# Performance work log

Hardware: AMD Instinct MI355X
Metric: run time of the kernel (lower is better)

The kernel has to match this reference:

```python
import jax, jax.numpy as jnp
import numpy as np

N, E = 50000, 800000          # nodes, edges
CUR, HID, OUT = 128, 128, 128  # cur_dim, hidden_dim, output_dim
NEG_SLOPE = 0.01               # F.leaky_relu default


def setup_inputs() -> dict:
    key = jax.random.key(0)
    ks = jax.random.split(key, 12)
    rn = lambda k, shp, s: jax.random.normal(k, shp, dtype=jnp.float32) * s
    s_c, s_h, s_o = 1.0 / np.sqrt(CUR), 1.0 / np.sqrt(HID), 1.0 / np.sqrt(OUT)
    return {
        "h": rn(ks[0], (N, CUR), 1.0),
        "x": rn(ks[1], (N, CUR), 1.0),
        "edge_index": jax.random.randint(ks[2], (2, E), 0, N, dtype=jnp.int32),
        "edge_weight": jax.random.uniform(ks[3], (E,), dtype=jnp.float32),
        # preprocessor_x: Linear(CUR, HID)
        "Wp": rn(ks[4], (HID, CUR), s_c), "bp": jnp.zeros((HID,), jnp.float32),
        # ChebConv(HID, OUT, K=2): two weight mats + bias
        "Wc0": rn(ks[5], (OUT, HID), s_h), "Wc1": rn(ks[6], (OUT, HID), s_h),
        "bc": jnp.zeros((OUT,), jnp.float32),
        # SAGEConv(HID, OUT): lin_rel (neighbors, with bias) + lin_root (self)
        "Wrel": rn(ks[7], (OUT, HID), s_h), "brel": jnp.zeros((OUT,), jnp.float32),
        "Wroot": rn(ks[8], (OUT, HID), s_h),
        # final Linear(OUT, OUT)
        "Wl": rn(ks[9], (OUT, OUT), s_o), "bl": jnp.zeros((OUT,), jnp.float32),
    }


def reference(h, x, edge_index, edge_weight, Wp, bp, Wc0, Wc1, bc,
              Wrel, brel, Wroot, Wl, bl):
    n = x.shape[0]
    src, dst = edge_index[0], edge_index[1]
    seg = lambda d, i: jax.ops.segment_sum(d, i, num_segments=n)

    his = x
    xh = x @ Wp.T + bp                               # [N, HID]

    # --- ChebConv, K=2, sym norm, lambda_max=2 => Lhat = -D^{-1/2} A D^{-1/2}
    deg = seg(edge_weight, src)                       # weighted degree
    dis = jnp.where(deg > 0, jax.lax.rsqrt(jnp.where(deg > 0, deg, 1.0)), 0.0)
    norm = -dis[src] * edge_weight * dis[dst]         # [E]
    Tx1 = seg(norm[:, None] * xh[src], dst)           # [N, HID]
    o1 = jax.nn.leaky_relu(xh @ Wc0.T + Tx1 @ Wc1.T + bc, NEG_SLOPE)

    # --- SAGEConv: mean of edge_weight-scaled neighbor feats + root transform
    msum = seg(edge_weight[:, None] * xh[src], dst)   # [N, HID]
    cnt = seg(jnp.ones_like(edge_weight), dst)        # in-degree
    mean = msum / jnp.maximum(cnt, 1.0)[:, None]
    o2 = jax.nn.leaky_relu(mean @ Wrel.T + brel + xh @ Wroot.T, NEG_SLOPE)

    o3 = (o1 + o2) @ Wl.T + bl
    return (his, o3)
```

## Files before the change

### kernel.cpp

```cpp
#include <hip/hip_runtime.h>

#define NN 50000
#define EE 800000
#define D  128
#define NCH 64
#define CH  12500
#define NR  8
#define RS  6250
#define KCB 512
#define KCB2 1024
#define XHB 782
#define CSB 196
#define PKB 384
#define FB  1563

typedef short short8 __attribute__((ext_vector_type(8)));
typedef float floatx4 __attribute__((ext_vector_type(4)));
typedef float floatx16 __attribute__((ext_vector_type(16)));

__device__ __forceinline__ float leaky(float v) { return v > 0.f ? v : 0.01f * v; }

__device__ __forceinline__ unsigned short f2bf(float f) {
    unsigned int u = __float_as_uint(f);
    u = (u + 0x7fff + ((u >> 16) & 1)) >> 16;
    return (unsigned short)u;
}
__device__ __forceinline__ float bf2f(unsigned int h) {
    return __uint_as_float(h << 16);
}

__global__ __launch_bounds__(256) void k_pre(
    const float* __restrict__ Wp,  const float* __restrict__ Wc0,
    const float* __restrict__ Wc1, const float* __restrict__ Wrel,
    const float* __restrict__ Wroot, const float* __restrict__ Wl,
    unsigned short* __restrict__ Pall) {
    int gid = blockIdx.x * 256 + threadIdx.x;
    int mm = gid >> 14;
    int r = gid & 16383;
    int j  = r & 7;
    int l  = (r >> 3) & 63;
    int n, k;
    if (mm == 0) {
        int ct = (r >> 9) & 7;
        int kc = r >> 12;
        n = ct * 16 + (l & 15);
        k = kc * 32 + (l >> 4) * 8 + j;
    } else {
        int ct = (r >> 9) & 3;
        int kc = (r >> 11) & 7;
        n = ct * 32 + (l & 31);
        k = kc * 16 + (l >> 5) * 8 + j;
    }
    const float* W = mm == 0 ? Wp : mm == 1 ? Wc0 : mm == 2 ? Wc1
                   : mm == 3 ? Wrel : mm == 4 ? Wroot : Wl;
    Pall[gid] = f2bf(W[n * 128 + k]);
}

__global__ __launch_bounds__(256) void k_main(
    const int* __restrict__ src, const int* __restrict__ dst,
    const float* __restrict__ ew,
    int* __restrict__ counts,
    float* __restrict__ degp,
    unsigned short* __restrict__ rank,
    const float* __restrict__ x, const float* __restrict__ bp,
    unsigned short* __restrict__ xh16, float* __restrict__ his,
    const unsigned short* __restrict__ Pall) {
    __shared__ __align__(16) unsigned int sbuf[6272];
    int b = blockIdx.x;
    if (b < KCB) {
        int c = b & 63;
        int rlo = (b >> 6) * RS;
        for (int i = threadIdx.x; i < RS / 2; i += 256) sbuf[i] = 0u;
        __syncthreads();
        int base = c * CH;
        for (int i0 = threadIdx.x * 4; i0 < CH; i0 += 1024) {
            int e = base + i0;
            int4 d4 = *(const int4*)(dst + e);
            unsigned dr;
            dr = (unsigned)(d4.x - rlo);
            if (dr < RS) {
                unsigned old = atomicAdd(&sbuf[dr >> 1], 1u << ((dr & 1) * 16));
                rank[e]     = (unsigned short)(old >> ((dr & 1) * 16));
            }
            dr = (unsigned)(d4.y - rlo);
            if (dr < RS) {
                unsigned old = atomicAdd(&sbuf[dr >> 1], 1u << ((dr & 1) * 16));
                rank[e + 1] = (unsigned short)(old >> ((dr & 1) * 16));
            }
            dr = (unsigned)(d4.z - rlo);
            if (dr < RS) {
                unsigned old = atomicAdd(&sbuf[dr >> 1], 1u << ((dr & 1) * 16));
                rank[e + 2] = (unsigned short)(old >> ((dr & 1) * 16));
            }
            dr = (unsigned)(d4.w - rlo);
            if (dr < RS) {
                unsigned old = atomicAdd(&sbuf[dr >> 1], 1u << ((dr & 1) * 16));
                rank[e + 3] = (unsigned short)(old >> ((dr & 1) * 16));
            }
        }
        __syncthreads();
        size_t ob = (size_t)c * NN + rlo;
        for (int i = threadIdx.x; i < RS; i += 256)
            counts[ob + i] = (int)((sbuf[i >> 1] >> ((i & 1) * 16)) & 0xffffu);
    } else if (b < KCB2) {
        int bb = b - KCB;
        int c = bb & 63;
        int rlo = (bb >> 6) * RS;
        float* sdeg = (float*)sbuf;
        for (int i = threadIdx.x; i < RS; i += 256) sdeg[i] = 0.f;
        __syncthreads();
        int base = c * CH;
        for (int i0 = threadIdx.x * 4; i0 < CH; i0 += 1024) {
            int e = base + i0;
            int4   s4 = *(const int4*)(src + e);
            float4 w4 = *(const float4*)(ew + e);
            unsigned sr;
            sr = (unsigned)(s4.x - rlo); if (sr < RS) atomicAdd(&sdeg[sr], w4.x);
            sr = (unsigned)(s4.y - rlo); if (sr < RS) atomicAdd(&sdeg[sr], w4.y);
            sr = (unsigned)(s4.z - rlo); if (sr < RS) atomicAdd(&sdeg[sr], w4.z);
            sr = (unsigned)(s4.w - rlo); if (sr < RS) atomicAdd(&sdeg[sr], w4.w);
        }
        __syncthreads();
        size_t ob = (size_t)c * NN + rlo;
        for (int i = threadIdx.x; i < RS; i += 256) degp[ob + i] = sdeg[i];
    } else {
        int bb = b - KCB2;
        const unsigned short* Pp = Pall;
        int wave = threadIdx.x >> 6, l = threadIdx.x & 63;
        int n0 = bb * 64 + wave * 16;
        int m = l & 15, q = l >> 4;
        int nodeA = n0 + m;
        bool av = nodeA < NN;
        int na = av ? nodeA : 0;
        floatx4 acc[8];
#pragma unroll
        for (int ct = 0; ct < 8; ++ct) acc[ct] = (floatx4)(0.f);
#pragma unroll
        for (int kc = 0; kc < 4; ++kc) {
            const float* ap = x + (size_t)na * 128 + kc * 32 + q * 8;
            float4 f0 = av ? *(const float4*)ap       : make_float4(0, 0, 0, 0);
            float4 f1 = av ? *(const float4*)(ap + 4) : make_float4(0, 0, 0, 0);
            if (av) {
                float* hp = his + (size_t)nodeA * 128 + kc * 32 + q * 8;
                *(float4*)hp       = f0;
                *(float4*)(hp + 4) = f1;
            }
            short8 a;
            a[0] = f2bf(f0.x); a[1] = f2bf(f0.y); a[2] = f2bf(f0.z); a[3] = f2bf(f0.w);
            a[4] = f2bf(f1.x); a[5] = f2bf(f1.y); a[6] = f2bf(f1.z); a[7] = f2bf(f1.w);
#pragma unroll
            for (int ct = 0; ct < 8; ++ct) {
                short8 bfr = *(const short8*)(Pp + ((kc * 8 + ct) << 9) + l * 8);
                acc[ct] = __builtin_amdgcn_mfma_f32_16x16x32_bf16(a, bfr, acc[ct], 0, 0, 0);
            }
        }
#pragma unroll
        for (int ct = 0; ct < 8; ++ct) {
            int col = ct * 16 + m;
            float bias = bp[col];
#pragma unroll
            for (int r = 0; r < 4; ++r) {
                int node = n0 + q * 4 + r;
                if (node < NN) xh16[(size_t)node * 128 + col] = f2bf(acc[ct][r] + bias);
            }
        }
    }
}

__global__ __launch_bounds__(256) void k_colscan(int* __restrict__ counts,
                                                 const float* __restrict__ degp,
                                                 int* __restrict__ cntI,
                                                 float* __restrict__ deg,
                                                 int* __restrict__ blocksum) {
    __shared__ int ws4[4];
    int t = threadIdx.x;
    int n = blockIdx.x * 256 + t;
    int acc = 0; float dacc = 0.f;
    if (n < NN) {
#pragma unroll 8
        for (int c = 0; c < NCH; ++c) {
            size_t idx = (size_t)c * NN + n;
            int v = counts[idx];
            counts[idx] = acc;
            acc += v;
            dacc += degp[idx];
        }
        cntI[n] = acc;
        deg[n] = dacc;
    }
    int s = (n < NN) ? acc : 0;
#pragma unroll
    for (int off = 32; off > 0; off >>= 1) s += __shfl_down(s, off, 64);
    if ((t & 63) == 0) ws4[t >> 6] = s;
    __syncthreads();
    if (t == 0) blocksum[blockIdx.x] = ws4[0] + ws4[1] + ws4[2] + ws4[3];
}

__global__ __launch_bounds__(256) void k_scan_mid(const int* __restrict__ blocksum,
                                                  int* __restrict__ blockoff,
                                                  int* __restrict__ rowstart) {
    __shared__ int wtot[4];
    int t = threadIdx.x, lane = t & 63, wave = t >> 6;
    int v = (t < CSB) ? blocksum[t] : 0;
    int incl = v;
#pragma unroll
    for (int off = 1; off < 64; off <<= 1) {
        int u = __shfl_up(incl, off, 64);
        if (lane >= off) incl += u;
    }
    if (lane == 63) wtot[wave] = incl;
    __syncthreads();
    int wpre = 0;
    for (int w = 0; w < wave; ++w) wpre += wtot[w];
    incl += wpre;
    if (t < CSB) blockoff[t] = incl - v;
    if (t == 255) rowstart[NN] = incl;
}

__global__ __launch_bounds__(256) void k_scan_final(const int* __restrict__ cntI,
                                                    const int* __restrict__ blockoff,
                                                    int* __restrict__ rowstart) {
    __shared__ int wtot[4];
    int t = threadIdx.x, lane = t & 63, wave = t >> 6;
    int n = blockIdx.x * 256 + t;
    int v = (n < NN) ? cntI[n] : 0;
    int incl = v;
#pragma unroll
    for (int off = 1; off < 64; off <<= 1) {
        int u = __shfl_up(incl, off, 64);
        if (lane >= off) incl += u;
    }
    if (lane == 63) wtot[wave] = incl;
    __syncthreads();
    int wpre = 0;
    for (int w = 0; w < wave; ++w) wpre += wtot[w];
    incl += wpre;
    if (n < NN) rowstart[n] = blockoff[blockIdx.x] + incl - v;
}

__global__ __launch_bounds__(256) void k_bucket(const int* __restrict__ src,
                                                const int* __restrict__ dst,
                                                const float* __restrict__ ew,
                                                const float* __restrict__ deg,
                                                const int* __restrict__ rowstart,
                                                const int* __restrict__ chunkoff,
                                                const unsigned short* __restrict__ rank,
                                                int4* __restrict__ rec) {
    int e = blockIdx.x * blockDim.x + threadIdx.x;
    if (e >= EE) return;
    int s = src[e], d = dst[e];
    float w = ew[e];
    float degs = deg[s];
    float dis_s = degs > 0.f ? rsqrtf(degs) : 0.f;
    int c = e / CH;
    int pos = rowstart[d] + chunkoff[(size_t)c * NN + d] + (int)rank[e];
    int4 r;
    r.x = s;
    r.y = __float_as_int(w);
    r.z = __float_as_int(dis_s * w);
    r.w = 0;
    rec[pos] = r;
}

__global__ __launch_bounds__(256) void k_gather(const int* __restrict__ rowstart,
                                                const int4* __restrict__ rec,
                                                const float* __restrict__ deg,
                                                const unsigned short* __restrict__ xh16,
                                                unsigned int* __restrict__ tx16,
                                                unsigned int* __restrict__ mn16) {
    int wave = threadIdx.x >> 6, l = threadIdx.x & 63;
    int n = blockIdx.x * 4 + wave;
    if (n >= NN) return;
    int lo = rowstart[n], hi = rowstart[n + 1];
    int half = l >> 5, c32 = l & 31;
    float am0 = 0.f, am1 = 0.f, am2 = 0.f, am3 = 0.f;
    float at0 = 0.f, at1 = 0.f, at2 = 0.f, at3 = 0.f;
    int e = lo + half;
    for (; e + 6 < hi; e += 8) {
        int4 r0 = rec[e], r1 = rec[e + 2], r2 = rec[e + 4], r3 = rec[e + 6];
        uint2 v0 = *(const uint2*)(xh16 + (size_t)r0.x * 128 + c32 * 4);
        uint2 v1 = *(const uint2*)(xh16 + (size_t)r1.x * 128 + c32 * 4);
        uint2 v2 = *(const uint2*)(xh16 + (size_t)r2.x * 128 + c32 * 4);
        uint2 v3 = *(const uint2*)(xh16 + (size_t)r3.x * 128 + c32 * 4);
        float w0 = __int_as_float(r0.y), u0 = __int_as_float(r0.z);
        float w1 = __int_as_float(r1.y), u1 = __int_as_float(r1.z);
        float w2 = __int_as_float(r2.y), u2 = __int_as_float(r2.z);
        float w3 = __int_as_float(r3.y), u3 = __int_as_float(r3.z);
        float a0, a1, a2, a3;
        a0 = bf2f(v0.x & 0xffff); a1 = bf2f(v0.x >> 16);
        a2 = bf2f(v0.y & 0xffff); a3 = bf2f(v0.y >> 16);
        am0 = fmaf(w0, a0, am0); am1 = fmaf(w0, a1, am1);
        am2 = fmaf(w0, a2, am2); am3 = fmaf(w0, a3, am3);
        at0 = fmaf(u0, a0, at0); at1 = fmaf(u0, a1, at1);
        at2 = fmaf(u0, a2, at2); at3 = fmaf(u0, a3, at3);
        a0 = bf2f(v1.x & 0xffff); a1 = bf2f(v1.x >> 16);
        a2 = bf2f(v1.y & 0xffff); a3 = bf2f(v1.y >> 16);
        am0 = fmaf(w1, a0, am0); am1 = fmaf(w1, a1, am1);
        am2 = fmaf(w1, a2, am2); am3 = fmaf(w1, a3, am3);
        at0 = fmaf(u1, a0, at0); at1 = fmaf(u1, a1, at1);
        at2 = fmaf(u1, a2, at2); at3 = fmaf(u1, a3, at3);
        a0 = bf2f(v2.x & 0xffff); a1 = bf2f(v2.x >> 16);
        a2 = bf2f(v2.y & 0xffff); a3 = bf2f(v2.y >> 16);
        am0 = fmaf(w2, a0, am0); am1 = fmaf(w2, a1, am1);
        am2 = fmaf(w2, a2, am2); am3 = fmaf(w2, a3, am3);
        at0 = fmaf(u2, a0, at0); at1 = fmaf(u2, a1, at1);
        at2 = fmaf(u2, a2, at2); at3 = fmaf(u2, a3, at3);
        a0 = bf2f(v3.x & 0xffff); a1 = bf2f(v3.x >> 16);
        a2 = bf2f(v3.y & 0xffff); a3 = bf2f(v3.y >> 16);
        am0 = fmaf(w3, a0, am0); am1 = fmaf(w3, a1, am1);
        am2 = fmaf(w3, a2, am2); am3 = fmaf(w3, a3, am3);
        at0 = fmaf(u3, a0, at0); at1 = fmaf(u3, a1, at1);
        at2 = fmaf(u3, a2, at2); at3 = fmaf(u3, a3, at3);
    }
    for (; e < hi; e += 2) {
        int4 r0 = rec[e];
        uint2 v0 = *(const uint2*)(xh16 + (size_t)r0.x * 128 + c32 * 4);
        float w0 = __int_as_float(r0.y), u0 = __int_as_float(r0.z);
        float a0 = bf2f(v0.x & 0xffff), a1 = bf2f(v0.x >> 16);
        float a2 = bf2f(v0.y & 0xffff), a3 = bf2f(v0.y >> 16);
        am0 = fmaf(w0, a0, am0); am1 = fmaf(w0, a1, am1);
        am2 = fmaf(w0, a2, am2); am3 = fmaf(w0, a3, am3);
        at0 = fmaf(u0, a0, at0); at1 = fmaf(u0, a1, at1);
        at2 = fmaf(u0, a2, at2); at3 = fmaf(u0, a3, at3);
    }
    am0 += __shfl_xor(am0, 32, 64); am1 += __shfl_xor(am1, 32, 64);
    am2 += __shfl_xor(am2, 32, 64); am3 += __shfl_xor(am3, 32, 64);
    at0 += __shfl_xor(at0, 32, 64); at1 += __shfl_xor(at1, 32, 64);
    at2 += __shfl_xor(at2, 32, 64); at3 += __shfl_xor(at3, 32, 64);
    float dd = deg[n];
    float dis_d = dd > 0.f ? rsqrtf(dd) : 0.f;
    int c = hi - lo;
    float ic = 1.f / (float)(c > 0 ? c : 1);
    if (half == 0) {
        uint2 t;
        t.x = (unsigned int)f2bf(-dis_d * at0) | ((unsigned int)f2bf(-dis_d * at1) << 16);
        t.y = (unsigned int)f2bf(-dis_d * at2) | ((unsigned int)f2bf(-dis_d * at3) << 16);
        *(uint2*)(tx16 + (size_t)n * 64 + c32 * 2) = t;
    } else {
        uint2 m;
        m.x = (unsigned int)f2bf(am0 * ic) | ((unsigned int)f2bf(am1 * ic) << 16);
        m.y = (unsigned int)f2bf(am2 * ic) | ((unsigned int)f2bf(am3 * ic) << 16);
        *(uint2*)(mn16 + (size_t)n * 64 + c32 * 2) = m;
    }
}

__global__ __launch_bounds__(256, 4) void k_fused(const unsigned short* __restrict__ xh16,
                                               const unsigned short* __restrict__ tx16,
                                               const unsigned short* __restrict__ mn16,
                                               const unsigned short* __restrict__ Pall,
                                               const float* __restrict__ bc,
                                               const float* __restrict__ brel,
                                               const float* __restrict__ bl,
                                               float* __restrict__ out) {
    const unsigned short* Pc0  = Pall + 1 * 16384;
    const unsigned short* Pc1  = Pall + 2 * 16384;
    const unsigned short* Prel = Pall + 3 * 16384;
    const unsigned short* Proot= Pall + 4 * 16384;
    const unsigned short* Pl   = Pall + 5 * 16384;
    __shared__ __align__(16) unsigned short sS[32][128];
    int ct = threadIdx.x >> 6, l = threadIdx.x & 63;
    int n0 = blockIdx.x * 32;
    int row = l & 31, half = l >> 5;
    int node = n0 + row;
    bool av = node < NN;
    size_t ra = (size_t)(av ? node : 0) * 128 + half * 8;
    floatx16 acc1 = (floatx16)(0.f), acc2 = (floatx16)(0.f);
#pragma unroll
    for (int kc = 0; kc < 8; ++kc) {
        short8 Axh = *(const short8*)(xh16 + ra + kc * 16);
        short8 Atx = *(const short8*)(tx16 + ra + kc * 16);
        short8 Amn = *(const short8*)(mn16 + ra + kc * 16);
        int po = ((kc * 4 + ct) << 9) + l * 8;
        short8 b0 = *(const short8*)(Pc0 + po);
        short8 b1 = *(const short8*)(Pc1 + po);
        short8 b2 = *(const short8*)(Prel + po);
        short8 b3 = *(const short8*)(Proot + po);
        acc1 = __builtin_amdgcn_mfma_f32_32x32x16_bf16(Axh, b0, acc1, 0, 0, 0);
        acc1 = __builtin_amdgcn_mfma_f32_32x32x16_bf16(Atx, b1, acc1, 0, 0, 0);
        acc2 = __builtin_amdgcn_mfma_f32_32x32x16_bf16(Amn, b2, acc2, 0, 0, 0);
        acc2 = __builtin_amdgcn_mfma_f32_32x32x16_bf16(Axh, b3, acc2, 0, 0, 0);
    }
    int col = ct * 32 + row;
    float b1v = bc[col], b2v = brel[col];
#pragma unroll
    for (int r = 0; r < 16; ++r) {
        int rr = (r & 3) + 8 * (r >> 2) + 4 * half;
        float u = leaky(acc1[r] + b1v) + leaky(acc2[r] + b2v);
        int sw = ((((col >> 3) ^ rr) & 15) << 3) | (col & 7);
        sS[rr][sw] = f2bf(u);
    }
    __syncthreads();
    floatx16 acc3 = (floatx16)(0.f);
#pragma unroll
    for (int kc = 0; kc < 8; ++kc) {
        int g = (kc * 2 + half) ^ (row & 15);
        short8 As = *(const short8*)&sS[row][g << 3];
        short8 b = *(const short8*)(Pl + ((kc * 4 + ct) << 9) + l * 8);
        acc3 = __builtin_amdgcn_mfma_f32_32x32x16_bf16(As, b, acc3, 0, 0, 0);
    }
    float bv = bl[col];
#pragma unroll
    for (int r = 0; r < 16; ++r) {
        int rr = (r & 3) + 8 * (r >> 2) + 4 * half;
        int nd = n0 + rr;
        if (nd < NN) out[(size_t)nd * 128 + col] = acc3[r] + bv;
    }
}

extern "C" void kernel_launch(void* const* d_in, const int* in_sizes, int n_in,
                              void* d_out, int out_size, void* d_ws, size_t ws_size,
                              hipStream_t stream) {
    const float* x    = (const float*)d_in[1];
    const int*   ei   = (const int*)d_in[2];
    const float* ew   = (const float*)d_in[3];
    const float* Wp   = (const float*)d_in[4];
    const float* bp   = (const float*)d_in[5];
    const float* Wc0  = (const float*)d_in[6];
    const float* Wc1  = (const float*)d_in[7];
    const float* bc   = (const float*)d_in[8];
    const float* Wrel = (const float*)d_in[9];
    const float* brel = (const float*)d_in[10];
    const float* Wroot= (const float*)d_in[11];
    const float* Wl   = (const float*)d_in[12];
    const float* bl   = (const float*)d_in[13];
    (void)in_sizes; (void)n_in; (void)out_size; (void)ws_size;
    float* out = (float*)d_out;

    unsigned short* xh16 = (unsigned short*)d_ws;
    unsigned short* tx16 = xh16 + (size_t)NN * 128;
    unsigned short* mn16 = tx16 + (size_t)NN * 128;
    unsigned short* Pall = mn16 + (size_t)NN * 128;
    int*   counts = (int*)(Pall + 6 * 16384);
    int4*  rec    = (int4*)(counts + (size_t)NCH * NN);
    float* degp   = (float*)rec;
    unsigned short* rank = (unsigned short*)(rec + EE);
    int*   rowstart = (int*)(rank + EE);
    int*   blocksum = rowstart + NN + 2;
    int*   blockoff = blocksum + CSB;
    int*   cntI   = blockoff + CSB;
    float* deg    = (float*)(cntI + NN);

    const int* srcI = ei;
    const int* dstI = ei + EE;

    k_pre<<<PKB, 256, 0, stream>>>(Wp, Wc0, Wc1, Wrel, Wroot, Wl, Pall);
    k_main<<<KCB2 + XHB, 256, 0, stream>>>(
        srcI, dstI, ew, counts, degp, rank, x, bp, xh16, out, Pall);
    k_colscan<<<CSB, 256, 0, stream>>>(counts, degp, cntI, deg, blocksum);
    k_scan_mid<<<1, 256, 0, stream>>>(blocksum, blockoff, rowstart);
    k_scan_final<<<CSB, 256, 0, stream>>>(cntI, blockoff, rowstart);
    k_bucket<<<(EE + 255) / 256, 256, 0, stream>>>(srcI, dstI, ew, deg, rowstart,
                                                   counts, rank, rec);
    k_gather<<<(NN + 3) / 4, 256, 0, stream>>>(rowstart, rec, deg, xh16,
                                               (unsigned int*)tx16, (unsigned int*)mn16);
    k_fused<<<FB, 256, 0, stream>>>(xh16, tx16, mn16, Pall,
                                    bc, brel, bl, out + (size_t)NN * 128);
}
```

Measured before the change: 246.1 us.

## Fuse neighbor gather into MFMA epilogue kernel and merge scan kernels

The CSR gather that builds the Chebyshev and mean-aggregated features now runs inside the fused MFMA kernel. Each block aggregates its 32 nodes into swizzled shared-memory tiles instead of writing tx16/mn16 to global memory and reading them back. Separately, the mid-level block-sum scan is folded into the final scan kernel, with every block redundantly scanning the 196 block sums. Together this drops two launches and one global round-trip of intermediate features. The cost is fewer waves doing the latency-bound gather per node, since 1563 blocks now each walk 8 nodes per wave serially, and extra shared memory that may lower occupancy.

```diff
diff --git a/kernel.cpp b/kernel.cpp
--- a/kernel.cpp
+++ b/kernel.cpp
@@ -196,12 +196,29 @@
     if (t == 0) blocksum[blockIdx.x] = ws4[0] + ws4[1] + ws4[2] + ws4[3];
 }
 
-__global__ __launch_bounds__(256) void k_scan_mid(const int* __restrict__ blocksum,
-                                                  int* __restrict__ blockoff,
-                                                  int* __restrict__ rowstart) {
+__global__ __launch_bounds__(256) void k_scan_final(const int* __restrict__ cntI,
+                                                    const int* __restrict__ blocksum,
+                                                    int* __restrict__ rowstart) {
+    __shared__ int sbs[256];
     __shared__ int wtot[4];
     int t = threadIdx.x, lane = t & 63, wave = t >> 6;
-    int v = (t < CSB) ? blocksum[t] : 0;
+    int bv = (t < CSB) ? blocksum[t] : 0;
+    int binc = bv;
+#pragma unroll
+    for (int off = 1; off < 64; off <<= 1) {
+        int u = __shfl_up(binc, off, 64);
+        if (lane >= off) binc += u;
+    }
+    if (lane == 63) wtot[wave] = binc;
+    __syncthreads();
+    int bpre = 0;
+    for (int w = 0; w < wave; ++w) bpre += wtot[w];
+    sbs[t] = binc + bpre;
+    __syncthreads();
+    int boff = (blockIdx.x == 0) ? 0 : sbs[blockIdx.x - 1];
+    if (blockIdx.x == 0 && t == 0) rowstart[NN] = sbs[CSB - 1];
+    int n = blockIdx.x * 256 + t;
+    int v = (n < NN) ? cntI[n] : 0;
     int incl = v;
 #pragma unroll
     for (int off = 1; off < 64; off <<= 1) {
@@ -213,29 +230,7 @@
     int wpre = 0;
     for (int w = 0; w < wave; ++w) wpre += wtot[w];
     incl += wpre;
-    if (t < CSB) blockoff[t] = incl - v;
-    if (t == 255) rowstart[NN] = incl;
-}
-
-__global__ __launch_bounds__(256) void k_scan_final(const int* __restrict__ cntI,
-                                                    const int* __restrict__ blockoff,
-                                                    int* __restrict__ rowstart) {
-    __shared__ int wtot[4];
-    int t = threadIdx.x, lane = t & 63, wave = t >> 6;
-    int n = blockIdx.x * 256 + t;
-    int v = (n < NN) ? cntI[n] : 0;
-    int incl = v;
-#pragma unroll
-    for (int off = 1; off < 64; off <<= 1) {
-        int u = __shfl_up(incl, off, 64);
-        if (lane >= off) incl += u;
-    }
-    if (lane == 63) wtot[wave] = incl;
-    __syncthreads();
-    int wpre = 0;
-    for (int w = 0; w < wave; ++w) wpre += wtot[w];
-    incl += wpre;
-    if (n < NN) rowstart[n] = blockoff[blockIdx.x] + incl - v;
+    if (n < NN) rowstart[n] = boff + incl - v;
 }
 
 __global__ __launch_bounds__(256) void k_bucket(const int* __restrict__ src,
@@ -262,91 +257,10 @@
     rec[pos] = r;
 }
 
-__global__ __launch_bounds__(256) void k_gather(const int* __restrict__ rowstart,
-                                                const int4* __restrict__ rec,
-                                                const float* __restrict__ deg,
-                                                const unsigned short* __restrict__ xh16,
-                                                unsigned int* __restrict__ tx16,
-                                                unsigned int* __restrict__ mn16) {
-    int wave = threadIdx.x >> 6, l = threadIdx.x & 63;
-    int n = blockIdx.x * 4 + wave;
-    if (n >= NN) return;
-    int lo = rowstart[n], hi = rowstart[n + 1];
-    int half = l >> 5, c32 = l & 31;
-    float am0 = 0.f, am1 = 0.f, am2 = 0.f, am3 = 0.f;
-    float at0 = 0.f, at1 = 0.f, at2 = 0.f, at3 = 0.f;
-    int e = lo + half;
-    for (; e + 6 < hi; e += 8) {
-        int4 r0 = rec[e], r1 = rec[e + 2], r2 = rec[e + 4], r3 = rec[e + 6];
-        uint2 v0 = *(const uint2*)(xh16 + (size_t)r0.x * 128 + c32 * 4);
-        uint2 v1 = *(const uint2*)(xh16 + (size_t)r1.x * 128 + c32 * 4);
-        uint2 v2 = *(const uint2*)(xh16 + (size_t)r2.x * 128 + c32 * 4);
-        uint2 v3 = *(const uint2*)(xh16 + (size_t)r3.x * 128 + c32 * 4);
-        float w0 = __int_as_float(r0.y), u0 = __int_as_float(r0.z);
-        float w1 = __int_as_float(r1.y), u1 = __int_as_float(r1.z);
-        float w2 = __int_as_float(r2.y), u2 = __int_as_float(r2.z);
-        float w3 = __int_as_float(r3.y), u3 = __int_as_float(r3.z);
-        float a0, a1, a2, a3;
-        a0 = bf2f(v0.x & 0xffff); a1 = bf2f(v0.x >> 16);
-        a2 = bf2f(v0.y & 0xffff); a3 = bf2f(v0.y >> 16);
-        am0 = fmaf(w0, a0, am0); am1 = fmaf(w0, a1, am1);
-        am2 = fmaf(w0, a2, am2); am3 = fmaf(w0, a3, am3);
-        at0 = fmaf(u0, a0, at0); at1 = fmaf(u0, a1, at1);
-        at2 = fmaf(u0, a2, at2); at3 = fmaf(u0, a3, at3);
-        a0 = bf2f(v1.x & 0xffff); a1 = bf2f(v1.x >> 16);
-        a2 = bf2f(v1.y & 0xffff); a3 = bf2f(v1.y >> 16);
-        am0 = fmaf(w1, a0, am0); am1 = fmaf(w1, a1, am1);
-        am2 = fmaf(w1, a2, am2); am3 = fmaf(w1, a3, am3);
-        at0 = fmaf(u1, a0, at0); at1 = fmaf(u1, a1, at1);
-        at2 = fmaf(u1, a2, at2); at3 = fmaf(u1, a3, at3);
-        a0 = bf2f(v2.x & 0xffff); a1 = bf2f(v2.x >> 16);
-        a2 = bf2f(v2.y & 0xffff); a3 = bf2f(v2.y >> 16);
-        am0 = fmaf(w2, a0, am0); am1 = fmaf(w2, a1, am1);
-        am2 = fmaf(w2, a2, am2); am3 = fmaf(w2, a3, am3);
-        at0 = fmaf(u2, a0, at0); at1 = fmaf(u2, a1, at1);
-        at2 = fmaf(u2, a2, at2); at3 = fmaf(u2, a3, at3);
-        a0 = bf2f(v3.x & 0xffff); a1 = bf2f(v3.x >> 16);
-        a2 = bf2f(v3.y & 0xffff); a3 = bf2f(v3.y >> 16);
-        am0 = fmaf(w3, a0, am0); am1 = fmaf(w3, a1, am1);
-        am2 = fmaf(w3, a2, am2); am3 = fmaf(w3, a3, am3);
-        at0 = fmaf(u3, a0, at0); at1 = fmaf(u3, a1, at1);
-        at2 = fmaf(u3, a2, at2); at3 = fmaf(u3, a3, at3);
-    }
-    for (; e < hi; e += 2) {
-        int4 r0 = rec[e];
-        uint2 v0 = *(const uint2*)(xh16 + (size_t)r0.x * 128 + c32 * 4);
-        float w0 = __int_as_float(r0.y), u0 = __int_as_float(r0.z);
-        float a0 = bf2f(v0.x & 0xffff), a1 = bf2f(v0.x >> 16);
-        float a2 = bf2f(v0.y & 0xffff), a3 = bf2f(v0.y >> 16);
-        am0 = fmaf(w0, a0, am0); am1 = fmaf(w0, a1, am1);
-        am2 = fmaf(w0, a2, am2); am3 = fmaf(w0, a3, am3);
-        at0 = fmaf(u0, a0, at0); at1 = fmaf(u0, a1, at1);
-        at2 = fmaf(u0, a2, at2); at3 = fmaf(u0, a3, at3);
-    }
-    am0 += __shfl_xor(am0, 32, 64); am1 += __shfl_xor(am1, 32, 64);
-    am2 += __shfl_xor(am2, 32, 64); am3 += __shfl_xor(am3, 32, 64);
-    at0 += __shfl_xor(at0, 32, 64); at1 += __shfl_xor(at1, 32, 64);
-    at2 += __shfl_xor(at2, 32, 64); at3 += __shfl_xor(at3, 32, 64);
-    float dd = deg[n];
-    float dis_d = dd > 0.f ? rsqrtf(dd) : 0.f;
-    int c = hi - lo;
-    float ic = 1.f / (float)(c > 0 ? c : 1);
-    if (half == 0) {
-        uint2 t;
-        t.x = (unsigned int)f2bf(-dis_d * at0) | ((unsigned int)f2bf(-dis_d * at1) << 16);
-        t.y = (unsigned int)f2bf(-dis_d * at2) | ((unsigned int)f2bf(-dis_d * at3) << 16);
-        *(uint2*)(tx16 + (size_t)n * 64 + c32 * 2) = t;
-    } else {
-        uint2 m;
-        m.x = (unsigned int)f2bf(am0 * ic) | ((unsigned int)f2bf(am1 * ic) << 16);
-        m.y = (unsigned int)f2bf(am2 * ic) | ((unsigned int)f2bf(am3 * ic) << 16);
-        *(uint2*)(mn16 + (size_t)n * 64 + c32 * 2) = m;
-    }
-}
-
-__global__ __launch_bounds__(256, 4) void k_fused(const unsigned short* __restrict__ xh16,
-                                               const unsigned short* __restrict__ tx16,
-                                               const unsigned short* __restrict__ mn16,
+__global__ __launch_bounds__(256, 4) void k_gf(const int* __restrict__ rowstart,
+                                               const int4* __restrict__ rec,
+                                               const float* __restrict__ deg,
+                                               const unsigned short* __restrict__ xh16,
                                                const unsigned short* __restrict__ Pall,
                                                const float* __restrict__ bc,
                                                const float* __restrict__ brel,
@@ -357,19 +271,102 @@
     const unsigned short* Prel = Pall + 3 * 16384;
     const unsigned short* Proot= Pall + 4 * 16384;
     const unsigned short* Pl   = Pall + 5 * 16384;
+    __shared__ __align__(16) unsigned short sTX[32][128];
+    __shared__ __align__(16) unsigned short sMN[32][128];
     __shared__ __align__(16) unsigned short sS[32][128];
-    int ct = threadIdx.x >> 6, l = threadIdx.x & 63;
+    int w = threadIdx.x >> 6, l = threadIdx.x & 63;
     int n0 = blockIdx.x * 32;
-    int row = l & 31, half = l >> 5;
+    int half = l >> 5, c32 = l & 31;
+    for (int i = 0; i < 8; ++i) {
+        int rr = w * 8 + i;
+        int n = n0 + rr;
+        int lo = 0, hi = 0;
+        if (n < NN) { lo = rowstart[n]; hi = rowstart[n + 1]; }
+        float am0 = 0.f, am1 = 0.f, am2 = 0.f, am3 = 0.f;
+        float at0 = 0.f, at1 = 0.f, at2 = 0.f, at3 = 0.f;
+        int e = lo + half;
+        for (; e + 6 < hi; e += 8) {
+            int4 r0 = rec[e], r1 = rec[e + 2], r2 = rec[e + 4], r3 = rec[e + 6];
+            uint2 v0 = *(const uint2*)(xh16 + (size_t)r0.x * 128 + c32 * 4);
+            uint2 v1 = *(const uint2*)(xh16 + (size_t)r1.x * 128 + c32 * 4);
+            uint2 v2 = *(const uint2*)(xh16 + (size_t)r2.x * 128 + c32 * 4);
+            uint2 v3 = *(const uint2*)(xh16 + (size_t)r3.x * 128 + c32 * 4);
+            float w0 = __int_as_float(r0.y), u0 = __int_as_float(r0.z);
+            float w1 = __int_as_float(r1.y), u1 = __int_as_float(r1.z);
+            float w2 = __int_as_float(r2.y), u2 = __int_as_float(r2.z);
+            float w3 = __int_as_float(r3.y), u3 = __int_as_float(r3.z);
+            float a0, a1, a2, a3;
+            a0 = bf2f(v0.x & 0xffff); a1 = bf2f(v0.x >> 16);
+            a2 = bf2f(v0.y & 0xffff); a3 = bf2f(v0.y >> 16);
+            am0 = fmaf(w0, a0, am0); am1 = fmaf(w0, a1, am1);
+            am2 = fmaf(w0, a2, am2); am3 = fmaf(w0, a3, am3);
+            at0 = fmaf(u0, a0, at0); at1 = fmaf(u0, a1, at1);
+            at2 = fmaf(u0, a2, at2); at3 = fmaf(u0, a3, at3);
+            a0 = bf2f(v1.x & 0xffff); a1 = bf2f(v1.x >> 16);
+            a2 = bf2f(v1.y & 0xffff); a3 = bf2f(v1.y >> 16);
+            am0 = fmaf(w1, a0, am0); am1 = fmaf(w1, a1, am1);
+            am2 = fmaf(w1, a2, am2); am3 = fmaf(w1, a3, am3);
+            at0 = fmaf(u1, a0, at0); at1 = fmaf(u1, a1, at1);
+            at2 = fmaf(u1, a2, at2); at3 = fmaf(u1, a3, at3);
+            a0 = bf2f(v2.x & 0xffff); a1 = bf2f(v2.x >> 16);
+            a2 = bf2f(v2.y & 0xffff); a3 = bf2f(v2.y >> 16);
+            am0 = fmaf(w2, a0, am0); am1 = fmaf(w2, a1, am1);
+            am2 = fmaf(w2, a2, am2); am3 = fmaf(w2, a3, am3);
+            at0 = fmaf(u2, a0, at0); at1 = fmaf(u2, a1, at1);
+            at2 = fmaf(u2, a2, at2); at3 = fmaf(u2, a3, at3);
+            a0 = bf2f(v3.x & 0xffff); a1 = bf2f(v3.x >> 16);
+            a2 = bf2f(v3.y & 0xffff); a3 = bf2f(v3.y >> 16);
+            am0 = fmaf(w3, a0, am0); am1 = fmaf(w3, a1, am1);
+            am2 = fmaf(w3, a2, am2); am3 = fmaf(w3, a3, am3);
+            at0 = fmaf(u3, a0, at0); at1 = fmaf(u3, a1, at1);
+            at2 = fmaf(u3, a2, at2); at3 = fmaf(u3, a3, at3);
+        }
+        for (; e < hi; e += 2) {
+            int4 r0 = rec[e];
+            uint2 v0 = *(const uint2*)(xh16 + (size_t)r0.x * 128 + c32 * 4);
+            float w0 = __int_as_float(r0.y), u0 = __int_as_float(r0.z);
+            float a0 = bf2f(v0.x & 0xffff), a1 = bf2f(v0.x >> 16);
+            float a2 = bf2f(v0.y & 0xffff), a3 = bf2f(v0.y >> 16);
+            am0 = fmaf(w0, a0, am0); am1 = fmaf(w0, a1, am1);
+            am2 = fmaf(w0, a2, am2); am3 = fmaf(w0, a3, am3);
+            at0 = fmaf(u0, a0, at0); at1 = fmaf(u0, a1, at1);
+            at2 = fmaf(u0, a2, at2); at3 = fmaf(u0, a3, at3);
+        }
+        am0 += __shfl_xor(am0, 32, 64); am1 += __shfl_xor(am1, 32, 64);
+        am2 += __shfl_xor(am2, 32, 64); am3 += __shfl_xor(am3, 32, 64);
+        at0 += __shfl_xor(at0, 32, 64); at1 += __shfl_xor(at1, 32, 64);
+        at2 += __shfl_xor(at2, 32, 64); at3 += __shfl_xor(at3, 32, 64);
+        float dd = (n < NN) ? deg[n] : 0.f;
+        float dis_d = dd > 0.f ? rsqrtf(dd) : 0.f;
+        int c = hi - lo;
+        float ic = 1.f / (float)(c > 0 ? c : 1);
+        int cb = c32 * 4;
+        int sw = ((((cb >> 3) ^ (rr & 15)) & 15) << 3) | (cb & 7);
+        if (half == 0) {
+            uint2 tv;
+            tv.x = (unsigned int)f2bf(-dis_d * at0) | ((unsigned int)f2bf(-dis_d * at1) << 16);
+            tv.y = (unsigned int)f2bf(-dis_d * at2) | ((unsigned int)f2bf(-dis_d * at3) << 16);
+            *(uint2*)&sTX[rr][sw] = tv;
+        } else {
+            uint2 mv;
+            mv.x = (unsigned int)f2bf(am0 * ic) | ((unsigned int)f2bf(am1 * ic) << 16);
+            mv.y = (unsigned int)f2bf(am2 * ic) | ((unsigned int)f2bf(am3 * ic) << 16);
+            *(uint2*)&sMN[rr][sw] = mv;
+        }
+    }
+    __syncthreads();
+    int ct = w;
+    int row = l & 31;
     int node = n0 + row;
     bool av = node < NN;
     size_t ra = (size_t)(av ? node : 0) * 128 + half * 8;
     floatx16 acc1 = (floatx16)(0.f), acc2 = (floatx16)(0.f);
 #pragma unroll
     for (int kc = 0; kc < 8; ++kc) {
+        int g = ((kc * 2 + half) ^ (row & 15)) & 15;
         short8 Axh = *(const short8*)(xh16 + ra + kc * 16);
-        short8 Atx = *(const short8*)(tx16 + ra + kc * 16);
-        short8 Amn = *(const short8*)(mn16 + ra + kc * 16);
+        short8 Atx = *(const short8*)&sTX[row][g << 3];
+        short8 Amn = *(const short8*)&sMN[row][g << 3];
         int po = ((kc * 4 + ct) << 9) + l * 8;
         short8 b0 = *(const short8*)(Pc0 + po);
         short8 b1 = *(const short8*)(Pc1 + po);
@@ -447,12 +444,9 @@
     k_main<<<KCB2 + XHB, 256, 0, stream>>>(
         srcI, dstI, ew, counts, degp, rank, x, bp, xh16, out, Pall);
     k_colscan<<<CSB, 256, 0, stream>>>(counts, degp, cntI, deg, blocksum);
-    k_scan_mid<<<1, 256, 0, stream>>>(blocksum, blockoff, rowstart);
-    k_scan_final<<<CSB, 256, 0, stream>>>(cntI, blockoff, rowstart);
+    k_scan_final<<<CSB, 256, 0, stream>>>(cntI, blocksum, rowstart);
     k_bucket<<<(EE + 255) / 256, 256, 0, stream>>>(srcI, dstI, ew, deg, rowstart,
                                                    counts, rank, rec);
-    k_gather<<<(NN + 3) / 4, 256, 0, stream>>>(rowstart, rec, deg, xh16,
-                                               (unsigned int*)tx16, (unsigned int*)mn16);
-    k_fused<<<FB, 256, 0, stream>>>(xh16, tx16, mn16, Pall,
-                                    bc, brel, bl, out + (size_t)NN * 128);
-}
+    k_gf<<<FB, 256, 0, stream>>>(rowstart, rec, deg, xh16, Pall,
+                                 bc, brel, bl, out + (size_t)NN * 128);
+}
```

New measurement: 257.3 us. +4.6%, slower.

## Pack per-chunk dst counters into 8-bit LDS slots and merge scan kernels

Applied to the files above, without the earlier changes.

The per-chunk destination counting now covers all 50000 nodes in one block per chunk, using 8-bit packed LDS counters instead of 16-bit counters split over eight row ranges. This cuts the number of blocks that each re-read the dst array. The two-level scan is also merged: every final-scan block recomputes the block-sum prefix itself, which removes one kernel launch. The risk is that 8-bit counters overflow if any node gets more than 255 edges from one 12500-edge chunk. There are also fewer blocks for the counting phase and larger LDS use per block, which lowers occupancy.

```diff
diff --git a/kernel.cpp b/kernel.cpp
--- a/kernel.cpp
+++ b/kernel.cpp
@@ -7,8 +7,8 @@
 #define CH  12500
 #define NR  8
 #define RS  6250
-#define KCB 512
-#define KCB2 1024
+#define KCA 64
+#define KAB 576
 #define XHB 782
 #define CSB 196
 #define PKB 384
@@ -65,45 +65,36 @@
     const float* __restrict__ x, const float* __restrict__ bp,
     unsigned short* __restrict__ xh16, float* __restrict__ his,
     const unsigned short* __restrict__ Pall) {
-    __shared__ __align__(16) unsigned int sbuf[6272];
+    __shared__ __align__(16) unsigned int sbuf[12544];
     int b = blockIdx.x;
-    if (b < KCB) {
-        int c = b & 63;
-        int rlo = (b >> 6) * RS;
-        for (int i = threadIdx.x; i < RS / 2; i += 256) sbuf[i] = 0u;
+    if (b < KCA) {
+        int c = b;
+        for (int i = threadIdx.x; i < 12500; i += 256) sbuf[i] = 0u;
         __syncthreads();
         int base = c * CH;
         for (int i0 = threadIdx.x * 4; i0 < CH; i0 += 1024) {
             int e = base + i0;
             int4 d4 = *(const int4*)(dst + e);
-            unsigned dr;
-            dr = (unsigned)(d4.x - rlo);
-            if (dr < RS) {
-                unsigned old = atomicAdd(&sbuf[dr >> 1], 1u << ((dr & 1) * 16));
-                rank[e]     = (unsigned short)(old >> ((dr & 1) * 16));
-            }
-            dr = (unsigned)(d4.y - rlo);
-            if (dr < RS) {
-                unsigned old = atomicAdd(&sbuf[dr >> 1], 1u << ((dr & 1) * 16));
-                rank[e + 1] = (unsigned short)(old >> ((dr & 1) * 16));
-            }
-            dr = (unsigned)(d4.z - rlo);
-            if (dr < RS) {
-                unsigned old = atomicAdd(&sbuf[dr >> 1], 1u << ((dr & 1) * 16));
-                rank[e + 2] = (unsigned short)(old >> ((dr & 1) * 16));
-            }
-            dr = (unsigned)(d4.w - rlo);
-            if (dr < RS) {
-                unsigned old = atomicAdd(&sbuf[dr >> 1], 1u << ((dr & 1) * 16));
-                rank[e + 3] = (unsigned short)(old >> ((dr & 1) * 16));
-            }
+            unsigned d, old;
+            d = (unsigned)d4.x;
+            old = atomicAdd(&sbuf[d >> 2], 1u << ((d & 3) * 8));
+            rank[e]     = (unsigned short)((old >> ((d & 3) * 8)) & 0xffu);
+            d = (unsigned)d4.y;
+            old = atomicAdd(&sbuf[d >> 2], 1u << ((d & 3) * 8));
+            rank[e + 1] = (unsigned short)((old >> ((d & 3) * 8)) & 0xffu);
+            d = (unsigned)d4.z;
+            old = atomicAdd(&sbuf[d >> 2], 1u << ((d & 3) * 8));
+            rank[e + 2] = (unsigned short)((old >> ((d & 3) * 8)) & 0xffu);
+            d = (unsigned)d4.w;
+            old = atomicAdd(&sbuf[d >> 2], 1u << ((d & 3) * 8));
+            rank[e + 3] = (unsigned short)((old >> ((d & 3) * 8)) & 0xffu);
         }
         __syncthreads();
-        size_t ob = (size_t)c * NN + rlo;
-        for (int i = threadIdx.x; i < RS; i += 256)
-            counts[ob + i] = (int)((sbuf[i >> 1] >> ((i & 1) * 16)) & 0xffffu);
-    } else if (b < KCB2) {
-        int bb = b - KCB;
+        size_t ob = (size_t)c * NN;
+        for (int i = threadIdx.x; i < NN; i += 256)
+            counts[ob + i] = (int)((sbuf[i >> 2] >> ((i & 3) * 8)) & 0xffu);
+    } else if (b < KAB) {
+        int bb = b - KCA;
         int c = bb & 63;
         int rlo = (bb >> 6) * RS;
         float* sdeg = (float*)sbuf;
@@ -124,7 +115,7 @@
         size_t ob = (size_t)c * NN + rlo;
         for (int i = threadIdx.x; i < RS; i += 256) degp[ob + i] = sdeg[i];
     } else {
-        int bb = b - KCB2;
+        int bb = b - KAB;
         const unsigned short* Pp = Pall;
         int wave = threadIdx.x >> 6, l = threadIdx.x & 63;
         int n0 = bb * 64 + wave * 16;
@@ -196,12 +187,29 @@
     if (t == 0) blocksum[blockIdx.x] = ws4[0] + ws4[1] + ws4[2] + ws4[3];
 }
 
-__global__ __launch_bounds__(256) void k_scan_mid(const int* __restrict__ blocksum,
-                                                  int* __restrict__ blockoff,
-                                                  int* __restrict__ rowstart) {
+__global__ __launch_bounds__(256) void k_scan_final(const int* __restrict__ cntI,
+                                                    const int* __restrict__ blocksum,
+                                                    int* __restrict__ rowstart) {
+    __shared__ int sbs[256];
     __shared__ int wtot[4];
     int t = threadIdx.x, lane = t & 63, wave = t >> 6;
-    int v = (t < CSB) ? blocksum[t] : 0;
+    int bv = (t < CSB) ? blocksum[t] : 0;
+    int binc = bv;
+#pragma unroll
+    for (int off = 1; off < 64; off <<= 1) {
+        int u = __shfl_up(binc, off, 64);
+        if (lane >= off) binc += u;
+    }
+    if (lane == 63) wtot[wave] = binc;
+    __syncthreads();
+    int bpre = 0;
+    for (int w = 0; w < wave; ++w) bpre += wtot[w];
+    sbs[t] = binc + bpre;
+    __syncthreads();
+    int boff = (blockIdx.x == 0) ? 0 : sbs[blockIdx.x - 1];
+    if (blockIdx.x == 0 && t == 0) rowstart[NN] = sbs[CSB - 1];
+    int n = blockIdx.x * 256 + t;
+    int v = (n < NN) ? cntI[n] : 0;
     int incl = v;
 #pragma unroll
     for (int off = 1; off < 64; off <<= 1) {
@@ -213,29 +221,7 @@
     int wpre = 0;
     for (int w = 0; w < wave; ++w) wpre += wtot[w];
     incl += wpre;
-    if (t < CSB) blockoff[t] = incl - v;
-    if (t == 255) rowstart[NN] = incl;
-}
-
-__global__ __launch_bounds__(256) void k_scan_final(const int* __restrict__ cntI,
-                                                    const int* __restrict__ blockoff,
-                                                    int* __restrict__ rowstart) {
-    __shared__ int wtot[4];
-    int t = threadIdx.x, lane = t & 63, wave = t >> 6;
-    int n = blockIdx.x * 256 + t;
-    int v = (n < NN) ? cntI[n] : 0;
-    int incl = v;
-#pragma unroll
-    for (int off = 1; off < 64; off <<= 1) {
-        int u = __shfl_up(incl, off, 64);
-        if (lane >= off) incl += u;
-    }
-    if (lane == 63) wtot[wave] = incl;
-    __syncthreads();
-    int wpre = 0;
-    for (int w = 0; w < wave; ++w) wpre += wtot[w];
-    incl += wpre;
-    if (n < NN) rowstart[n] = blockoff[blockIdx.x] + incl - v;
+    if (n < NN) rowstart[n] = boff + incl - v;
 }
 
 __global__ __launch_bounds__(256) void k_bucket(const int* __restrict__ src,
@@ -444,11 +430,10 @@
     const int* dstI = ei + EE;
 
     k_pre<<<PKB, 256, 0, stream>>>(Wp, Wc0, Wc1, Wrel, Wroot, Wl, Pall);
-    k_main<<<KCB2 + XHB, 256, 0, stream>>>(
+    k_main<<<KAB + XHB, 256, 0, stream>>>(
         srcI, dstI, ew, counts, degp, rank, x, bp, xh16, out, Pall);
     k_colscan<<<CSB, 256, 0, stream>>>(counts, degp, cntI, deg, blocksum);
-    k_scan_mid<<<1, 256, 0, stream>>>(blocksum, blockoff, rowstart);
-    k_scan_final<<<CSB, 256, 0, stream>>>(cntI, blockoff, rowstart);
+    k_scan_final<<<CSB, 256, 0, stream>>>(cntI, blocksum, rowstart);
     k_bucket<<<(EE + 255) / 256, 256, 0, stream>>>(srcI, dstI, ew, deg, rowstart,
                                                    counts, rank, rec);
     k_gather<<<(NN + 3) / 4, 256, 0, stream>>>(rowstart, rec, deg, xh16,
```

After: 253.0 us. 2.8% more time.
